# Kernel optimization log

Hardware: AMD Instinct MI355X
Metric: run time of the kernel (lower is better)

Reference implementation:

```python
import jax, jax.numpy as jnp
import numpy as np

N = 50000   # nodes
E = 640000  # edges
IN = 128
HID = 128
EPS = 1e-5


def setup_inputs() -> dict:
    key = jax.random.key(0)
    ks = jax.random.split(key, 8)
    s = 1.0 / np.sqrt(IN)
    inp = {
        "x": jax.random.normal(ks[0], (N, IN), jnp.float32),
        "src": jax.random.randint(ks[1], (E,), 0, N, dtype=jnp.int32),
        "dst": jax.random.randint(ks[2], (E,), 0, N, dtype=jnp.int32),
        "W1": jax.random.normal(ks[3], (IN, HID), jnp.float32) * s,
        "b1": jnp.zeros((HID,), jnp.float32),
        "g1": jnp.ones((HID,), jnp.float32),
        "be1": jnp.zeros((HID,), jnp.float32),
        "W2": jax.random.normal(ks[4], (HID, HID), jnp.float32) * s,
        "b2": jnp.zeros((HID,), jnp.float32),
        "g2": jnp.ones((HID,), jnp.float32),
        "be2": jnp.zeros((HID,), jnp.float32),
        "W3": jax.random.normal(ks[5], (HID, HID), jnp.float32) * s,
        "b3": jnp.zeros((HID,), jnp.float32),
        "g3": jnp.ones((HID,), jnp.float32),
        "be3": jnp.zeros((HID,), jnp.float32),
    }
    return inp


def _layernorm(h, g, b):
    mu = jnp.mean(h, axis=-1, keepdims=True)
    var = jnp.mean(jnp.square(h - mu), axis=-1, keepdims=True)
    return g * (h - mu) * jax.lax.rsqrt(var + EPS) + b


def _gcn_conv(h, W, b, src, dst):
    # Kipf & Welling GCN: D^{-1/2} (A + I) D^{-1/2} (H W) + b
    # self-loops added with weight 1; degree computed on the target index.
    hw = h @ W                                          # [N, HID]
    deg = jax.ops.segment_sum(jnp.ones((E,), h.dtype), dst, num_segments=N) + 1.0
    dinv = jax.lax.rsqrt(deg)                           # deg >= 1 due to self loop
    msg = hw[src] * (dinv[src] * dinv[dst])[:, None]    # gather + normalize, [E, HID]
    agg = jax.ops.segment_sum(msg, dst, num_segments=N)  # scatter-add
    agg = agg + hw * (dinv * dinv)[:, None]             # self-loop contribution
    return agg + b


def reference(x, src, dst, W1, b1, g1, be1, W2, b2, g2, be2, W3, b3, g3, be3):
    layers = [(W1, b1, g1, be1), (W2, b2, g2, be2), (W3, b3, g3, be3)]
    h = x
    for i, (W, b, g, be) in enumerate(layers):
        h_in = h
        h = _gcn_conv(h, W, b, src, dst)
        h = _layernorm(h, g, be)
        h = jax.nn.relu(h)
        # dropout: eval mode -> identity
        if i > 0 and h.shape == h_in.shape:
            h = h + h_in
    return h
```

## Files before the change

kernel.cpp:

```cpp
#include <hip/hip_runtime.h>
#include <hip/hip_bf16.h>

#define NFEAT 128
#define EPSLN 1e-5f
#define PAD 64

typedef __attribute__((ext_vector_type(8))) short short8;
typedef __attribute__((ext_vector_type(4))) float f32x4;

__device__ __forceinline__ float bf2f(ushort u) {
    union { uint u32; float f; } v; v.u32 = ((uint)u) << 16; return v.f;
}
__device__ __forceinline__ ushort f2bf(float f) {
    union { float f; uint u32; } v; v.f = f;
    uint u = v.u32;
    u += 0x7FFF + ((u >> 16) & 1);
    return (ushort)(u >> 16);
}

__global__ void setup_kernel(int4* __restrict__ cnt4, int ncnt4,
                             ushort* __restrict__ hwb_padrow,
                             const float* __restrict__ W0, const float* __restrict__ W1,
                             const float* __restrict__ W2,
                             ushort* __restrict__ Wt0, ushort* __restrict__ Wt1,
                             ushort* __restrict__ Wt2) {
    int i = blockIdx.x * 256 + threadIdx.x;
    if (i < ncnt4) cnt4[i] = make_int4(0, 0, 0, 0);
    if (i < 16) ((uint4*)hwb_padrow)[i] = make_uint4(0, 0, 0, 0);
    if (i < 3 * NFEAT * NFEAT) {
        int l = i / (NFEAT * NFEAT);
        int r = i - l * (NFEAT * NFEAT);
        int k = r >> 7, n = r & 127;
        const float* W = (l == 0) ? W0 : (l == 1) ? W1 : W2;
        ushort* Wt = (l == 0) ? Wt0 : (l == 1) ? Wt1 : Wt2;
        Wt[n * NFEAT + k] = f2bf(W[r]);
    }
}

__global__ void fill_kernel(const int* __restrict__ src, const int* __restrict__ dst,
                            int* __restrict__ cnt, int* __restrict__ csr, int E) {
    int e = blockIdx.x * 256 + threadIdx.x;
    if (e < E) {
        int d = dst[e];
        int s = src[e];
        int pos = atomicAdd(&cnt[d], 1);
        if (pos < PAD) csr[d * PAD + pos] = s;
    }
}

__global__ __launch_bounds__(256) void gemm_mfma_kernel(const ushort* __restrict__ hb,
                                                        const float* __restrict__ hf,
                                                        const ushort* __restrict__ Wt,
                                                        const int* __restrict__ cnt,
                                                        ushort* __restrict__ hw, int N) {
    __shared__ ushort WtL[NFEAT * NFEAT];
    {
        const uint4* src4 = (const uint4*)Wt;
        uint4* dst4 = (uint4*)WtL;
        #pragma unroll
        for (int i = 0; i < 8; ++i)
            dst4[threadIdx.x + i * 256] = src4[threadIdx.x + i * 256];
    }
    __syncthreads();

    const int wave = threadIdx.x >> 6;
    const int lane = threadIdx.x & 63;
    const int quad = lane >> 4;
    const int l16  = lane & 15;
    const int row0 = blockIdx.x * 128 + wave * 32;

    short8 afrag[2][4];
    #pragma unroll
    for (int t = 0; t < 2; ++t) {
        const int arow = row0 + t * 16 + l16;
        const bool rowok = (arow < N);
        if (hf) {
            const float4* fp = (const float4*)(hf + (size_t)arow * NFEAT);
            #pragma unroll
            for (int ks = 0; ks < 4; ++ks) {
                short8 a = short8{0, 0, 0, 0, 0, 0, 0, 0};
                if (rowok) {
                    float4 u0 = fp[ks * 8 + quad * 2];
                    float4 u1 = fp[ks * 8 + quad * 2 + 1];
                    a[0] = (short)f2bf(u0.x); a[1] = (short)f2bf(u0.y);
                    a[2] = (short)f2bf(u0.z); a[3] = (short)f2bf(u0.w);
                    a[4] = (short)f2bf(u1.x); a[5] = (short)f2bf(u1.y);
                    a[6] = (short)f2bf(u1.z); a[7] = (short)f2bf(u1.w);
                }
                afrag[t][ks] = a;
            }
        } else {
            const short8* ap = (const short8*)(hb + (size_t)arow * NFEAT);
            #pragma unroll
            for (int ks = 0; ks < 4; ++ks) {
                if (rowok) afrag[t][ks] = ap[ks * 4 + quad];
                else       afrag[t][ks] = short8{0, 0, 0, 0, 0, 0, 0, 0};
            }
        }
    }

    f32x4 acc[2][8];
    #pragma unroll
    for (int t = 0; t < 2; ++t)
        #pragma unroll
        for (int ct = 0; ct < 8; ++ct) acc[t][ct] = f32x4{0.f, 0.f, 0.f, 0.f};

    #pragma unroll
    for (int ct = 0; ct < 8; ++ct) {
        const int bcol = ct * 16 + l16;
        const short8* bp = (const short8*)(WtL + (size_t)bcol * NFEAT);
        #pragma unroll
        for (int ks = 0; ks < 4; ++ks) {
            short8 bfrag = bp[ks * 4 + quad];
            acc[0][ct] = __builtin_amdgcn_mfma_f32_16x16x32_bf16(afrag[0][ks], bfrag, acc[0][ct], 0, 0, 0);
            acc[1][ct] = __builtin_amdgcn_mfma_f32_16x16x32_bf16(afrag[1][ks], bfrag, acc[1][ct], 0, 0, 0);
        }
    }

    __syncthreads();
    ushort* tb = WtL + wave * (32 * NFEAT);

    #pragma unroll
    for (int t = 0; t < 2; ++t) {
        #pragma unroll
        for (int r = 0; r < 4; ++r) {
            const int rl = t * 16 + quad * 4 + r;
            const int orow = row0 + rl;
            const float di = (orow < N) ? rsqrtf((float)cnt[orow] + 1.0f) : 0.f;
            #pragma unroll
            for (int ct = 0; ct < 8; ++ct)
                tb[rl * NFEAT + ct * 16 + l16] = f2bf(acc[t][ct][r] * di);
        }
    }
    #pragma unroll
    for (int i = 0; i < 8; ++i) {
        const int c = i * 64 + lane;
        const int rl = c >> 4;
        const int ch = c & 15;
        const int orow = row0 + rl;
        uint4 v = *(const uint4*)(tb + rl * NFEAT + ch * 8);
        if (orow < N)
            ((uint4*)(hw + (size_t)orow * NFEAT))[ch] = v;
    }
}

__global__ __launch_bounds__(256) void agg_ln_kernel(const ushort* __restrict__ hwb,
                                                     const int* __restrict__ cnt,
                                                     const int* __restrict__ csr,
                                                     const float* __restrict__ bias,
                                                     const float* __restrict__ gamma,
                                                     const float* __restrict__ beta,
                                                     const ushort* __restrict__ hres_b,
                                                     float* __restrict__ outf,
                                                     ushort* __restrict__ outb,
                                                     int N) {
    const int node = blockIdx.x * 4 + (threadIdx.x >> 6);
    const int lane = threadIdx.x & 63;
    if (node >= N) return;
    const int quad = lane >> 4;
    const int l16  = lane & 15;
    const int c0i  = l16 * 8;

    const int cn  = cnt[node];
    const int deg = (cn < PAD) ? cn : PAD;
    const float di = rsqrtf((float)cn + 1.0f);
    const int* ce = csr + (size_t)node * PAD;
    const uint4* hw4 = (const uint4*)hwb;

    int myidx = (lane < deg) ? ce[lane] : N;
    uint4 hv = hw4[(size_t)node * 16 + l16];

    float acc[8];
    #pragma unroll
    for (int i = 0; i < 8; ++i) acc[i] = 0.f;

    const int ng = (deg + 15) >> 4;
    for (int gi = 0; gi < ng; ++gi) {
        const int jb = gi * 16 + quad;
        const int s0 = __shfl(myidx, jb);
        const int s1 = __shfl(myidx, jb + 4);
        const int s2 = __shfl(myidx, jb + 8);
        const int s3 = __shfl(myidx, jb + 12);
        uint4 v0 = hw4[(size_t)s0 * 16 + l16];
        uint4 v1 = hw4[(size_t)s1 * 16 + l16];
        uint4 v2 = hw4[(size_t)s2 * 16 + l16];
        uint4 v3 = hw4[(size_t)s3 * 16 + l16];
        acc[0] += bf2f((ushort)(v0.x & 0xFFFF)) + bf2f((ushort)(v1.x & 0xFFFF))
                + bf2f((ushort)(v2.x & 0xFFFF)) + bf2f((ushort)(v3.x & 0xFFFF));
        acc[1] += bf2f((ushort)(v0.x >> 16)) + bf2f((ushort)(v1.x >> 16))
                + bf2f((ushort)(v2.x >> 16)) + bf2f((ushort)(v3.x >> 16));
        acc[2] += bf2f((ushort)(v0.y & 0xFFFF)) + bf2f((ushort)(v1.y & 0xFFFF))
                + bf2f((ushort)(v2.y & 0xFFFF)) + bf2f((ushort)(v3.y & 0xFFFF));
        acc[3] += bf2f((ushort)(v0.y >> 16)) + bf2f((ushort)(v1.y >> 16))
                + bf2f((ushort)(v2.y >> 16)) + bf2f((ushort)(v3.y >> 16));
        acc[4] += bf2f((ushort)(v0.z & 0xFFFF)) + bf2f((ushort)(v1.z & 0xFFFF))
                + bf2f((ushort)(v2.z & 0xFFFF)) + bf2f((ushort)(v3.z & 0xFFFF));
        acc[5] += bf2f((ushort)(v0.z >> 16)) + bf2f((ushort)(v1.z >> 16))
                + bf2f((ushort)(v2.z >> 16)) + bf2f((ushort)(v3.z >> 16));
        acc[6] += bf2f((ushort)(v0.w & 0xFFFF)) + bf2f((ushort)(v1.w & 0xFFFF))
                + bf2f((ushort)(v2.w & 0xFFFF)) + bf2f((ushort)(v3.w & 0xFFFF));
        acc[7] += bf2f((ushort)(v0.w >> 16)) + bf2f((ushort)(v1.w >> 16))
                + bf2f((ushort)(v2.w >> 16)) + bf2f((ushort)(v3.w >> 16));
    }

    #pragma unroll
    for (int i = 0; i < 8; ++i) {
        acc[i] += __shfl_xor(acc[i], 16);
        acc[i] += __shfl_xor(acc[i], 32);
    }

    float4 b0 = ((const float4*)(bias + c0i))[0];
    float4 b1 = ((const float4*)(bias + c0i))[1];
    float xv[8];
    xv[0] = (acc[0] + bf2f((ushort)(hv.x & 0xFFFF))) * di + b0.x;
    xv[1] = (acc[1] + bf2f((ushort)(hv.x >> 16)))   * di + b0.y;
    xv[2] = (acc[2] + bf2f((ushort)(hv.y & 0xFFFF))) * di + b0.z;
    xv[3] = (acc[3] + bf2f((ushort)(hv.y >> 16)))   * di + b0.w;
    xv[4] = (acc[4] + bf2f((ushort)(hv.z & 0xFFFF))) * di + b1.x;
    xv[5] = (acc[5] + bf2f((ushort)(hv.z >> 16)))   * di + b1.y;
    xv[6] = (acc[6] + bf2f((ushort)(hv.w & 0xFFFF))) * di + b1.z;
    xv[7] = (acc[7] + bf2f((ushort)(hv.w >> 16)))   * di + b1.w;

    float s = 0.f, sq = 0.f;
    #pragma unroll
    for (int i = 0; i < 8; ++i) { s += xv[i]; sq += xv[i] * xv[i]; }
    #pragma unroll
    for (int o = 8; o > 0; o >>= 1) {
        s  += __shfl_xor(s, o);
        sq += __shfl_xor(sq, o);
    }
    const float mu  = s * (1.0f / NFEAT);
    const float var = sq * (1.0f / NFEAT) - mu * mu;
    const float rs  = rsqrtf(var + EPSLN);

    float4 g0 = ((const float4*)(gamma + c0i))[0];
    float4 g1 = ((const float4*)(gamma + c0i))[1];
    float4 e0 = ((const float4*)(beta + c0i))[0];
    float4 e1 = ((const float4*)(beta + c0i))[1];
    float gm[8] = {g0.x, g0.y, g0.z, g0.w, g1.x, g1.y, g1.z, g1.w};
    float bt[8] = {e0.x, e0.y, e0.z, e0.w, e1.x, e1.y, e1.z, e1.w};

    float y[8];
    #pragma unroll
    for (int i = 0; i < 8; ++i)
        y[i] = fmaxf(gm[i] * (xv[i] - mu) * rs + bt[i], 0.0f);

    if (hres_b) {
        uint4 hr = ((const uint4*)hres_b)[(size_t)node * 16 + l16];
        y[0] += bf2f((ushort)(hr.x & 0xFFFF));
        y[1] += bf2f((ushort)(hr.x >> 16));
        y[2] += bf2f((ushort)(hr.y & 0xFFFF));
        y[3] += bf2f((ushort)(hr.y >> 16));
        y[4] += bf2f((ushort)(hr.z & 0xFFFF));
        y[5] += bf2f((ushort)(hr.z >> 16));
        y[6] += bf2f((ushort)(hr.w & 0xFFFF));
        y[7] += bf2f((ushort)(hr.w >> 16));
    }

    if (quad == 0) {
        if (outf) {
            float4* op = (float4*)(outf + (size_t)node * NFEAT + c0i);
            op[0] = make_float4(y[0], y[1], y[2], y[3]);
            op[1] = make_float4(y[4], y[5], y[6], y[7]);
        }
        if (outb) {
            uint4 ob;
            ob.x = (uint)f2bf(y[0]) | ((uint)f2bf(y[1]) << 16);
            ob.y = (uint)f2bf(y[2]) | ((uint)f2bf(y[3]) << 16);
            ob.z = (uint)f2bf(y[4]) | ((uint)f2bf(y[5]) << 16);
            ob.w = (uint)f2bf(y[6]) | ((uint)f2bf(y[7]) << 16);
            ((uint4*)outb)[(size_t)node * 16 + l16] = ob;
        }
    }
}

extern "C" void kernel_launch(void* const* d_in, const int* in_sizes, int n_in,
                              void* d_out, int out_size, void* d_ws, size_t ws_size,
                              hipStream_t stream) {
    const float* x   = (const float*)d_in[0];
    const int*   src = (const int*)d_in[1];
    const int*   dst = (const int*)d_in[2];
    const float* W[3]  = {(const float*)d_in[3], (const float*)d_in[7],  (const float*)d_in[11]};
    const float* b[3]  = {(const float*)d_in[4], (const float*)d_in[8],  (const float*)d_in[12]};
    const float* g[3]  = {(const float*)d_in[5], (const float*)d_in[9],  (const float*)d_in[13]};
    const float* be[3] = {(const float*)d_in[6], (const float*)d_in[10], (const float*)d_in[14]};

    const int N = in_sizes[0] / NFEAT;
    const int E = in_sizes[1];

    char* ws = (char*)d_ws;
    size_t off = 0;
    auto carve = [&](size_t bytes) -> char* {
        char* p = ws + off;
        off = (off + bytes + 255) & ~(size_t)255;
        return p;
    };
    const int ncnt4 = (N + 3) / 4;
    int*    cnt = (int*)   carve((size_t)ncnt4 * 4 * sizeof(int));
    int*    csr = (int*)   carve(((size_t)N * PAD + 64) * sizeof(int));
    ushort* hwb = (ushort*)carve((size_t)(N + 1) * NFEAT * sizeof(ushort));
    ushort* h1b = (ushort*)carve((size_t)N * NFEAT * sizeof(ushort));
    ushort* h2b = (ushort*)carve((size_t)N * NFEAT * sizeof(ushort));
    ushort* Wt[3];
    for (int l = 0; l < 3; ++l) Wt[l] = (ushort*)carve(NFEAT * NFEAT * sizeof(ushort));
    (void)ws_size;

    int setup_threads = 3 * NFEAT * NFEAT;
    if (ncnt4 > setup_threads) setup_threads = ncnt4;
    setup_kernel<<<(setup_threads + 255) / 256, 256, 0, stream>>>(
        (int4*)cnt, ncnt4, hwb + (size_t)N * NFEAT,
        W[0], W[1], W[2], Wt[0], Wt[1], Wt[2]);

    fill_kernel<<<(E + 255) / 256, 256, 0, stream>>>(src, dst, cnt, csr, E);

    const ushort* hbin[3]  = {nullptr, h1b, h2b};
    const float*  hfin[3]  = {x, nullptr, nullptr};
    const ushort* hresb[3] = {nullptr, h1b, h2b};
    float*        houtf[3] = {nullptr, nullptr, (float*)d_out};
    ushort*       houtb[3] = {h1b, h2b, nullptr};

    const int gemm_blocks = (N + 127) / 128;
    const int agg_blocks = (N + 3) / 4;

    for (int l = 0; l < 3; ++l) {
        gemm_mfma_kernel<<<gemm_blocks, 256, 0, stream>>>(hbin[l], hfin[l], Wt[l], cnt, hwb, N);
        agg_ln_kernel<<<agg_blocks, 256, 0, stream>>>(hwb, cnt, csr,
                                                      b[l], g[l], be[l],
                                                      hresb[l], houtf[l], houtb[l], N);
    }
}
```

Measured before the change: 264.8 us.

## Process four nodes per wave in aggregation, one 16-lane group per node

Result: faster. 256.2 us (-3.2%).

```diff
diff --git a/kernel.cpp b/kernel.cpp
--- a/kernel.cpp
+++ b/kernel.cpp
@@ -154,33 +154,47 @@
                                                      float* __restrict__ outf,
                                                      ushort* __restrict__ outb,
                                                      int N) {
-    const int node = blockIdx.x * 4 + (threadIdx.x >> 6);
     const int lane = threadIdx.x & 63;
-    if (node >= N) return;
-    const int quad = lane >> 4;
+    const int wave = threadIdx.x >> 6;
+    const int grp  = lane >> 4;
     const int l16  = lane & 15;
     const int c0i  = l16 * 8;
 
-    const int cn  = cnt[node];
-    const int deg = (cn < PAD) ? cn : PAD;
-    const float di = rsqrtf((float)cn + 1.0f);
+    int node = blockIdx.x * 16 + wave * 4 + grp;
+    const bool ok = (node < N);
+    if (!ok) node = N - 1;
+
     const int* ce = csr + (size_t)node * PAD;
     const uint4* hw4 = (const uint4*)hwb;
 
-    int myidx = (lane < deg) ? ce[lane] : N;
+    int4 myidx4 = ((const int4*)ce)[l16];
+    const int cn = cnt[node];
     uint4 hv = hw4[(size_t)node * 16 + l16];
+    uint4 hr = make_uint4(0, 0, 0, 0);
+    if (hres_b) hr = ((const uint4*)hres_b)[(size_t)node * 16 + l16];
+
+    const int deg = (cn < PAD) ? cn : PAD;
+
+    int ng = (deg + 3) >> 2;
+    { int t = __shfl_xor(ng, 16); ng = (t > ng) ? t : ng; }
+    { int t = __shfl_xor(ng, 32); ng = (t > ng) ? t : ng; }
 
     float acc[8];
     #pragma unroll
     for (int i = 0; i < 8; ++i) acc[i] = 0.f;
 
-    const int ng = (deg + 15) >> 4;
-    for (int gi = 0; gi < ng; ++gi) {
-        const int jb = gi * 16 + quad;
-        const int s0 = __shfl(myidx, jb);
-        const int s1 = __shfl(myidx, jb + 4);
-        const int s2 = __shfl(myidx, jb + 8);
-        const int s3 = __shfl(myidx, jb + 12);
+    const int grpbase = lane & 48;
+    for (int it = 0; it < ng; ++it) {
+        const int sl = grpbase + it;
+        int t0 = __shfl(myidx4.x, sl);
+        int t1 = __shfl(myidx4.y, sl);
+        int t2 = __shfl(myidx4.z, sl);
+        int t3 = __shfl(myidx4.w, sl);
+        const int e0 = it * 4;
+        const int s0 = (e0     < deg) ? t0 : N;
+        const int s1 = (e0 + 1 < deg) ? t1 : N;
+        const int s2 = (e0 + 2 < deg) ? t2 : N;
+        const int s3 = (e0 + 3 < deg) ? t3 : N;
         uint4 v0 = hw4[(size_t)s0 * 16 + l16];
         uint4 v1 = hw4[(size_t)s1 * 16 + l16];
         uint4 v2 = hw4[(size_t)s2 * 16 + l16];
@@ -203,11 +217,7 @@
                 + bf2f((ushort)(v2.w >> 16)) + bf2f((ushort)(v3.w >> 16));
     }
 
-    #pragma unroll
-    for (int i = 0; i < 8; ++i) {
-        acc[i] += __shfl_xor(acc[i], 16);
-        acc[i] += __shfl_xor(acc[i], 32);
-    }
+    const float di = rsqrtf((float)cn + 1.0f);
 
     float4 b0 = ((const float4*)(bias + c0i))[0];
     float4 b1 = ((const float4*)(bias + c0i))[1];
@@ -246,7 +256,6 @@
         y[i] = fmaxf(gm[i] * (xv[i] - mu) * rs + bt[i], 0.0f);
 
     if (hres_b) {
-        uint4 hr = ((const uint4*)hres_b)[(size_t)node * 16 + l16];
         y[0] += bf2f((ushort)(hr.x & 0xFFFF));
         y[1] += bf2f((ushort)(hr.x >> 16));
         y[2] += bf2f((ushort)(hr.y & 0xFFFF));
@@ -257,7 +266,7 @@
         y[7] += bf2f((ushort)(hr.w >> 16));
     }
 
-    if (quad == 0) {
+    if (ok) {
         if (outf) {
             float4* op = (float4*)(outf + (size_t)node * NFEAT + c0i);
             op[0] = make_float4(y[0], y[1], y[2], y[3]);
@@ -320,7 +329,7 @@
     ushort*       houtb[3] = {h1b, h2b, nullptr};
 
     const int gemm_blocks = (N + 127) / 128;
-    const int agg_blocks = (N + 3) / 4;
+    const int agg_blocks = (N + 15) / 16;
 
     for (int l = 0; l < 3; ++l) {
         gemm_mfma_kernel<<<gemm_blocks, 256, 0, stream>>>(hbin[l], hfin[l], Wt[l], cnt, hwb, N);
```
